# Optimization experiments

Hardware: AMD Instinct MI355X
Metric: run time of the kernel (lower is better)

Reference implementation:

```python
import jax, jax.numpy as jnp
import numpy as np

B, T, IN, H, NB, OUT = 256, 2048, 128, 256, 4, 8
BS = H // NB  # branch size = 64


def setup_inputs() -> dict:
    key = jax.random.key(0)
    ks = jax.random.split(key, 7)
    x = jax.random.normal(ks[0], (B, T, IN), dtype=jnp.float32)
    Wb = jax.random.normal(ks[1], (NB, IN, BS), dtype=jnp.float32) * (1.0 / np.sqrt(IN))
    bb = jax.random.normal(ks[2], (NB, BS), dtype=jnp.float32) * 0.05
    Wo = jax.random.normal(ks[3], (H, OUT), dtype=jnp.float32) * (1.0 / np.sqrt(H))
    bo = jax.random.normal(ks[4], (OUT,), dtype=jnp.float32) * 0.05
    # tau_m ~ U(0,4); tau_n branch i ~ U(-4+2i, -1+2i) per the torch init
    tau_m = jax.random.uniform(ks[5], (H,), dtype=jnp.float32, minval=0.0, maxval=4.0)
    lo = (-4.0 + 2.0 * jnp.arange(NB, dtype=jnp.float32))[:, None]
    tau_n = lo + 3.0 * jax.random.uniform(ks[6], (NB, BS), dtype=jnp.float32)
    return {"x": x, "Wb": Wb, "bb": bb, "Wo": Wo, "bo": bo,
            "tau_m": tau_m, "tau_n": tau_n}


def reference(x, Wb, bb, Wo, bo, tau_m, tau_n):
    Bsz = x.shape[0]
    # Batch all per-step branch projections into one einsum: [B,T,NB,BS] -> [B,T,H]
    # (branch i writes slice [i*BS:(i+1)*BS], which matches the reshape order)
    D = jnp.einsum('bti,nis->btns', x, Wb) + bb  # [B,T,NB,BS]
    D = D.reshape(Bsz, x.shape[1], -1)           # [B,T,H]

    beta = jax.nn.sigmoid(tau_n).reshape(-1)     # [H], per-branch smoothing
    alpha = jax.nn.sigmoid(tau_m)                # [H]

    def step(carry, d_t):
        c, m = carry
        c = beta * c + (1.0 - beta) * d_t        # dendritic current EMA
        m = alpha * m + (1.0 - alpha) * c        # membrane EMA
        o = jax.nn.sigmoid(m @ Wo + bo)          # [B,OUT]
        return (c, m), o

    init = (jnp.zeros((Bsz, D.shape[-1]), D.dtype),
            jnp.zeros((Bsz, D.shape[-1]), D.dtype))
    _, outs = jax.lax.scan(step, init, jnp.swapaxes(D, 0, 1))  # outs: [T,B,OUT]
    return jnp.swapaxes(outs, 0, 1)              # [B,T,OUT]
```

## Files before the change

kernel.cpp:

```cpp
#include <hip/hip_runtime.h>
#include <hip/hip_bf16.h>
#include <math.h>

#define DEVFN __device__ __forceinline__

typedef __attribute__((ext_vector_type(8))) __bf16 bf16x8;
typedef __attribute__((ext_vector_type(8))) short s16x8;
typedef __attribute__((ext_vector_type(4))) float f32x4;
typedef __attribute__((ext_vector_type(4))) unsigned int u32x4;

constexpr int Tt    = 2048;
constexpr int INt   = 128;
constexpr int Ht    = 256;
constexpr int OUTt  = 8;
constexpr int TT    = 32;
constexpr int NTILE = 64;

union Frag {
  s16x8 s;
  bf16x8 b;
  u32x4 u;
};

DEVFN unsigned short f2bf(float f) {
  unsigned int u = __builtin_bit_cast(unsigned int, f);
  u += 0x7fffu + ((u >> 16) & 1u);
  return (unsigned short)(u >> 16);
}

DEVFN unsigned int pack2(float lo, float hi) {
  return (unsigned int)f2bf(lo) | ((unsigned int)f2bf(hi) << 16);
}

__global__
__attribute__((amdgpu_flat_work_group_size(1024, 1024)))
void sfnn_fused(
    const float* __restrict__ x, const float* __restrict__ Wb,
    const float* __restrict__ bb, const float* __restrict__ Wo,
    const float* __restrict__ bo, const float* __restrict__ tau_m,
    const float* __restrict__ tau_n, float* __restrict__ out)
{
  const int b    = blockIdx.x;
  const int tid  = threadIdx.x;
  const int lane = tid & 63;
  const int w    = tid >> 6;
  const int l16  = lane & 15;
  const int lhi  = lane >> 4;
  const int sid  = tid - 512;

  __shared__ __align__(16) unsigned char  Xb[3][TT * 256];
  __shared__ __align__(16) float          DfT[2][Ht * TT];
  __shared__ __align__(16) unsigned short Mb[2][TT * Ht];
  __shared__ __align__(16) unsigned short WoT[16 * Ht];

  {
    const int j  = w;
    const int k0 = 4 * (tid & 63);
    float v0 = 0.f, v1 = 0.f, v2 = 0.f, v3 = 0.f;
    if (j < OUTt) {
      v0 = Wo[(k0 + 0) * OUTt + j]; v1 = Wo[(k0 + 1) * OUTt + j];
      v2 = Wo[(k0 + 2) * OUTt + j]; v3 = Wo[(k0 + 3) * OUTt + j];
    }
    unsigned long long pk = (unsigned long long)pack2(v0, v1) |
                            ((unsigned long long)pack2(v2, v3) << 32);
    *(unsigned long long*)(&WoT[j * 256 + (k0 ^ ((j & 7) << 3))]) = pk;
  }

  Frag Wf[4];
  {
    const int h = 16 * w + l16;
    const int n = h >> 6, s = h & 63;
    #pragma unroll
    for (int ks = 0; ks < 4; ++ks) {
      #pragma unroll
      for (int j = 0; j < 8; ++j) {
        const int i = 32 * ks + 8 * lhi + j;
        Wf[ks].s[j] = (short)f2bf(Wb[(n * 128 + i) * 64 + s]);
      }
    }
  }

  float beta = 0.f, alpha = 0.f, omb = 0.f, oma = 0.f, bbh = 0.f;
  if (tid < 256) {
    beta  = 1.f / (1.f + expf(-tau_n[tid]));
    alpha = 1.f / (1.f + expf(-tau_m[tid]));
    omb   = 1.f - beta;
    oma   = 1.f - alpha;
    bbh   = bb[tid];
  }
  float bo_l = 0.f;
  if (w == 4 || w == 5) bo_l = (l16 < OUTt) ? bo[l16] : 0.f;

  const float* xb   = x   + (size_t)b * Tt * INt;
  float*       outb = out + (size_t)b * Tt * OUTt;

  float c_s = 0.f, m_s = 0.f;
  f32x4 dacc[2];
  f32x4 QA0, QA1, QB0, QB1;

  #define BAR() do {                                                       \
    asm volatile("s_waitcnt lgkmcnt(0)" ::: "memory");                     \
    __builtin_amdgcn_s_barrier();                                          \
  } while (0)

  #define WAITVM(N) do {                                                   \
    asm volatile("s_waitcnt vmcnt(" #N ")" ::: "memory");                  \
    __builtin_amdgcn_sched_barrier(0);                                     \
  } while (0)

  #define ISSUE(TILE, Q0, Q1) do {                                         \
    const float* _p = xb + (size_t)(TILE) * (TT * INt) + 4 * (size_t)sid;  \
    asm volatile("global_load_dwordx4 %0, %1, off" : "=&v"(Q0) : "v"(_p));        \
    asm volatile("global_load_dwordx4 %0, %1, off" : "=&v"(Q1) : "v"(_p + 2048)); \
  } while (0)

  #define STAGEWR(BUF, Q0, Q1) do {                                        \
    const int kb = 8 * (sid & 31);                                         \
    {                                                                      \
      const int t = (sid >> 5);                                            \
      unsigned long long pk = (unsigned long long)pack2(Q0.x, Q0.y) |      \
            ((unsigned long long)pack2(Q0.z, Q0.w) << 32);                 \
      *(unsigned long long*)(&Xb[BUF][t * 256 + (kb ^ ((t & 7) << 4))]) = pk; \
    }                                                                      \
    {                                                                      \
      const int t = 16 + (sid >> 5);                                       \
      unsigned long long pk = (unsigned long long)pack2(Q1.x, Q1.y) |      \
            ((unsigned long long)pack2(Q1.z, Q1.w) << 32);                 \
      *(unsigned long long*)(&Xb[BUF][t * 256 + (kb ^ ((t & 7) << 4))]) = pk; \
    }                                                                      \
  } while (0)

  #define GEMM(BUF) do {                                                   \
    _Pragma("unroll")                                                      \
    for (int tt = 0; tt < 2; ++tt) {                                       \
      dacc[tt] = f32x4{0.f, 0.f, 0.f, 0.f};                                \
      const int row = 16 * tt + l16;                                       \
      const int rs = row * 256, sw = (row & 7) << 4;                       \
      _Pragma("unroll")                                                    \
      for (int ks = 0; ks < 4; ++ks) {                                     \
        Frag a;                                                            \
        a.u = *(const u32x4*)(&Xb[BUF][rs + ((64 * ks + 16 * lhi) ^ sw)]); \
        dacc[tt] = __builtin_amdgcn_mfma_f32_16x16x32_bf16(                \
            a.b, Wf[ks].b, dacc[tt], 0, 0, 0);                             \
      }                                                                    \
    }                                                                      \
  } while (0)

  #define WRITEDF(BUF) do {                                                \
    const int h = 16 * w + l16;                                            \
    _Pragma("unroll")                                                      \
    for (int tt = 0; tt < 2; ++tt) {                                       \
      const int qi = 4 * tt + lhi;                                         \
      *(f32x4*)(&DfT[BUF][h * 32 + ((qi ^ (h & 7)) << 2)]) = dacc[tt];     \
    }                                                                      \
  } while (0)

  #define SCAN(BUF) do {                                                   \
    if (tid < 256) {                                                       \
      const int hb = tid * 32, h7 = tid & 7;                               \
      _Pragma("unroll")                                                    \
      for (int g = 0; g < 2; ++g) {                                        \
        f32x4 dv[4];                                                       \
        _Pragma("unroll")                                                  \
        for (int q = 0; q < 4; ++q)                                        \
          dv[q] = *(const f32x4*)(&DfT[BUF][hb + (((4 * g + q) ^ h7) << 2)]); \
        _Pragma("unroll")                                                  \
        for (int q = 0; q < 4; ++q)                                        \
          _Pragma("unroll")                                                \
          for (int r = 0; r < 4; ++r) {                                    \
            const int t = 16 * g + 4 * q + r;                              \
            const float d = dv[q][r] + bbh;                                \
            c_s = fmaf(beta, c_s, omb * d);                                \
            m_s = fmaf(alpha, m_s, oma * c_s);                             \
            Mb[BUF][t * 256 + (tid ^ ((t & 7) << 3))] = f2bf(m_s);         \
          }                                                                \
      }                                                                    \
    }                                                                      \
  } while (0)

  #define PROJ(TI, BUF) do {                                               \
    const int tp = w - 4;                                                  \
    const int trow = 16 * tp + l16;                                        \
    const int mrb = trow * 256, msw = (trow & 7) << 3;                     \
    const int wrb = l16 * 256,  wsw = (l16 & 7) << 3;                      \
    f32x4 p = f32x4{0.f, 0.f, 0.f, 0.f};                                   \
    _Pragma("unroll")                                                      \
    for (int ks = 0; ks < 8; ++ks) {                                       \
      const int k0 = 32 * ks + 8 * lhi;                                    \
      Frag ma, wo;                                                         \
      ma.u = *(const u32x4*)(&Mb[BUF][mrb + (k0 ^ msw)]);                  \
      wo.u = *(const u32x4*)(&WoT[wrb + (k0 ^ wsw)]);                      \
      p = __builtin_amdgcn_mfma_f32_16x16x32_bf16(ma.b, wo.b, p, 0, 0, 0); \
    }                                                                      \
    if (l16 < OUTt) {                                                      \
      _Pragma("unroll")                                                    \
      for (int r = 0; r < 4; ++r) {                                        \
        const int t = 16 * tp + 4 * lhi + r;                               \
        outb[(size_t)((TI) * TT + t) * OUTt + l16] =                       \
            1.f / (1.f + __expf(-(p[r] + bo_l)));                          \
      }                                                                    \
    }                                                                      \
  } while (0)

  #define ITER_EV(I, DOG, DOS, DOP, DOISS, DOSTG, WN) do {                 \
    if ((DOISS) && w >= 8) ISSUE((I) + 2, QA0, QA1);                       \
    if (DOG) { GEMM((I) % 3); WRITEDF((I) & 1); }                          \
    if ((DOS) && w < 4) SCAN(((I) - 1) & 1);                               \
    if ((DOP) && (w == 4 || w == 5)) PROJ((I) - 2, (I) & 1);               \
    if ((DOSTG) && w >= 8) { WAITVM(WN); STAGEWR(((I) + 1) % 3, QB0, QB1); } \
    BAR();                                                                 \
  } while (0)

  #define ITER_OD(I, DOG, DOS, DOP, DOISS, DOSTG, WN) do {                 \
    if ((DOISS) && w >= 8) ISSUE((I) + 2, QB0, QB1);                       \
    if (DOG) { GEMM((I) % 3); WRITEDF((I) & 1); }                          \
    if ((DOS) && w < 4) SCAN(((I) - 1) & 1);                               \
    if ((DOP) && (w == 4 || w == 5)) PROJ((I) - 2, (I) & 1);               \
    if ((DOSTG) && w >= 8) { WAITVM(WN); STAGEWR(((I) + 1) % 3, QA0, QA1); } \
    BAR();                                                                 \
  } while (0)

  if (w >= 8) {
    ISSUE(0, QA0, QA1);
    WAITVM(0);
    STAGEWR(0, QA0, QA1);
    ISSUE(1, QB0, QB1);
  }
  BAR();

  ITER_EV(0, 1, 0, 0, 1, 1, 2);
  ITER_OD(1, 1, 1, 0, 1, 1, 2);
  for (int jj = 1; jj <= 30; ++jj) {
    ITER_EV(2 * jj,     1, 1, 1, 1, 1, 2);
    ITER_OD(2 * jj + 1, 1, 1, 1, 1, 1, 2);
  }
  ITER_EV(62, 1, 1, 1, 0, 1, 0);
  ITER_OD(63, 1, 1, 1, 0, 0, 0);
  ITER_EV(64, 0, 1, 1, 0, 0, 0);
  ITER_OD(65, 0, 0, 1, 0, 0, 0);

  #undef ISSUE
  #undef STAGEWR
  #undef GEMM
  #undef WRITEDF
  #undef SCAN
  #undef PROJ
  #undef ITER_EV
  #undef ITER_OD
  #undef BAR
  #undef WAITVM
}

extern "C" void kernel_launch(void* const* d_in, const int* in_sizes, int n_in,
                              void* d_out, int out_size, void* d_ws, size_t ws_size,
                              hipStream_t stream) {
  const float* x     = (const float*)d_in[0];
  const float* Wb    = (const float*)d_in[1];
  const float* bb    = (const float*)d_in[2];
  const float* Wo    = (const float*)d_in[3];
  const float* bo    = (const float*)d_in[4];
  const float* tau_m = (const float*)d_in[5];
  const float* tau_n = (const float*)d_in[6];
  float* out = (float*)d_out;

  sfnn_fused<<<dim3(256), dim3(1024), 0, stream>>>(x, Wb, bb, Wo, bo, tau_m, tau_n, out);
}
```

Measured before the change: 96.59 us.

## Stream x tiles via direct-to-LDS DMA and specialize waves by role

Two dedicated loader waves now copy raw fp32 x tiles straight into a double-buffered LDS staging area with global_load_lds. They then convert each tile to swizzled bf16 in a separate LDS buffer. The GEMM moves off all 16 waves onto 8 waves, each computing two 16-column N tiles with reused A fragments, and the Xb ring drops from three buffers to two. The aim is to cut register-staged loads and per-wave overhead, and to separate scan, projection, GEMM and loading into disjoint wave roles. In exchange, LDS use rises to about 152KB and global load bandwidth depends on only two waves.

```diff
diff --git a/kernel.cpp b/kernel.cpp
--- a/kernel.cpp
+++ b/kernel.cpp
@@ -30,6 +30,15 @@
 
 DEVFN unsigned int pack2(float lo, float hi) {
   return (unsigned int)f2bf(lo) | ((unsigned int)f2bf(hi) << 16);
+}
+
+typedef __attribute__((address_space(3))) unsigned int lds_u32;
+typedef const __attribute__((address_space(1))) unsigned int glb_u32;
+
+DEVFN void dma16(const float* g, const float* l) {
+  __builtin_amdgcn_global_load_lds((glb_u32*)(uintptr_t)g,
+                                   (lds_u32*)(unsigned int)(uintptr_t)l,
+                                   16, 0, 0);
 }
 
 __global__
@@ -46,9 +55,12 @@
   const int w    = tid >> 6;
   const int l16  = lane & 15;
   const int lhi  = lane >> 4;
-  const int sid  = tid - 512;
-
-  __shared__ __align__(16) unsigned char  Xb[3][TT * 256];
+
+  const int hg  = w - 6;
+  const int sw2 = w - 14;
+
+  __shared__ __align__(16) float          Xraw[2][TT * INt];
+  __shared__ __align__(16) unsigned char  Xb[2][TT * 256];
   __shared__ __align__(16) float          DfT[2][Ht * TT];
   __shared__ __align__(16) unsigned short Mb[2][TT * Ht];
   __shared__ __align__(16) unsigned short WoT[16 * Ht];
@@ -66,16 +78,19 @@
     *(unsigned long long*)(&WoT[j * 256 + (k0 ^ ((j & 7) << 3))]) = pk;
   }
 
-  Frag Wf[4];
-  {
-    const int h = 16 * w + l16;
-    const int n = h >> 6, s = h & 63;
+  Frag Wf[2][4];
+  if (w >= 6 && w < 14) {
     #pragma unroll
-    for (int ks = 0; ks < 4; ++ks) {
+    for (int nh = 0; nh < 2; ++nh) {
+      const int h = 32 * hg + 16 * nh + l16;
+      const int n = h >> 6, s = h & 63;
       #pragma unroll
-      for (int j = 0; j < 8; ++j) {
-        const int i = 32 * ks + 8 * lhi + j;
-        Wf[ks].s[j] = (short)f2bf(Wb[(n * 128 + i) * 64 + s]);
+      for (int ks = 0; ks < 4; ++ks) {
+        #pragma unroll
+        for (int j = 0; j < 8; ++j) {
+          const int i = 32 * ks + 8 * lhi + j;
+          Wf[nh][ks].s[j] = (short)f2bf(Wb[(n * 128 + i) * 64 + s]);
+        }
       }
     }
   }
@@ -95,8 +110,7 @@
   float*       outb = out + (size_t)b * Tt * OUTt;
 
   float c_s = 0.f, m_s = 0.f;
-  f32x4 dacc[2];
-  f32x4 QA0, QA1, QB0, QB1;
+  f32x4 dacc[2][2];
 
   #define BAR() do {                                                       \
     asm volatile("s_waitcnt lgkmcnt(0)" ::: "memory");                     \
@@ -108,50 +122,58 @@
     __builtin_amdgcn_sched_barrier(0);                                     \
   } while (0)
 
-  #define ISSUE(TILE, Q0, Q1) do {                                         \
-    const float* _p = xb + (size_t)(TILE) * (TT * INt) + 4 * (size_t)sid;  \
-    asm volatile("global_load_dwordx4 %0, %1, off" : "=&v"(Q0) : "v"(_p));        \
-    asm volatile("global_load_dwordx4 %0, %1, off" : "=&v"(Q1) : "v"(_p + 2048)); \
-  } while (0)
-
-  #define STAGEWR(BUF, Q0, Q1) do {                                        \
-    const int kb = 8 * (sid & 31);                                         \
-    {                                                                      \
-      const int t = (sid >> 5);                                            \
-      unsigned long long pk = (unsigned long long)pack2(Q0.x, Q0.y) |      \
-            ((unsigned long long)pack2(Q0.z, Q0.w) << 32);                 \
-      *(unsigned long long*)(&Xb[BUF][t * 256 + (kb ^ ((t & 7) << 4))]) = pk; \
-    }                                                                      \
-    {                                                                      \
-      const int t = 16 + (sid >> 5);                                       \
-      unsigned long long pk = (unsigned long long)pack2(Q1.x, Q1.y) |      \
-            ((unsigned long long)pack2(Q1.z, Q1.w) << 32);                 \
-      *(unsigned long long*)(&Xb[BUF][t * 256 + (kb ^ ((t & 7) << 4))]) = pk; \
+  #define ISSUE_DMA(TILE) do {                                             \
+    const int _bi = (TILE) & 1;                                            \
+    const float* _gs = xb + (size_t)(TILE) * (TT * INt);                   \
+    _Pragma("unroll")                                                      \
+    for (int q = 0; q < 8; ++q) {                                          \
+      const int c = 8 * sw2 + q;                                           \
+      dma16(_gs + c * 256 + lane * 4, &Xraw[_bi][c * 256]);                \
+    }                                                                      \
+  } while (0)
+
+  #define CONVERT(TILE) do {                                               \
+    const int _bi = (TILE) & 1;                                            \
+    const int kb  = 8 * (lane & 31);                                       \
+    _Pragma("unroll")                                                      \
+    for (int q = 0; q < 8; ++q) {                                          \
+      const int c = 8 * sw2 + q;                                           \
+      const int t = 2 * c + (lane >> 5);                                   \
+      f32x4 v = *(const f32x4*)(&Xraw[_bi][256 * c + 4 * lane]);           \
+      unsigned long long pk = (unsigned long long)pack2(v[0], v[1]) |      \
+            ((unsigned long long)pack2(v[2], v[3]) << 32);                 \
+      *(unsigned long long*)(&Xb[_bi][t * 256 + (kb ^ ((t & 7) << 4))]) = pk; \
     }                                                                      \
   } while (0)
 
   #define GEMM(BUF) do {                                                   \
     _Pragma("unroll")                                                      \
     for (int tt = 0; tt < 2; ++tt) {                                       \
-      dacc[tt] = f32x4{0.f, 0.f, 0.f, 0.f};                                \
+      _Pragma("unroll")                                                    \
+      for (int nh = 0; nh < 2; ++nh) dacc[tt][nh] = f32x4{0.f,0.f,0.f,0.f};\
       const int row = 16 * tt + l16;                                       \
       const int rs = row * 256, sw = (row & 7) << 4;                       \
       _Pragma("unroll")                                                    \
       for (int ks = 0; ks < 4; ++ks) {                                     \
         Frag a;                                                            \
         a.u = *(const u32x4*)(&Xb[BUF][rs + ((64 * ks + 16 * lhi) ^ sw)]); \
-        dacc[tt] = __builtin_amdgcn_mfma_f32_16x16x32_bf16(                \
-            a.b, Wf[ks].b, dacc[tt], 0, 0, 0);                             \
+        _Pragma("unroll")                                                  \
+        for (int nh = 0; nh < 2; ++nh)                                     \
+          dacc[tt][nh] = __builtin_amdgcn_mfma_f32_16x16x32_bf16(          \
+              a.b, Wf[nh][ks].b, dacc[tt][nh], 0, 0, 0);                   \
       }                                                                    \
     }                                                                      \
   } while (0)
 
   #define WRITEDF(BUF) do {                                                \
-    const int h = 16 * w + l16;                                            \
     _Pragma("unroll")                                                      \
     for (int tt = 0; tt < 2; ++tt) {                                       \
       const int qi = 4 * tt + lhi;                                         \
-      *(f32x4*)(&DfT[BUF][h * 32 + ((qi ^ (h & 7)) << 2)]) = dacc[tt];     \
+      _Pragma("unroll")                                                    \
+      for (int nh = 0; nh < 2; ++nh) {                                     \
+        const int h = 32 * hg + 16 * nh + l16;                             \
+        *(f32x4*)(&DfT[BUF][h * 32 + ((qi ^ (h & 7)) << 2)]) = dacc[tt][nh]; \
+      }                                                                    \
     }                                                                      \
   } while (0)
 
@@ -202,51 +224,38 @@
     }                                                                      \
   } while (0)
 
-  #define ITER_EV(I, DOG, DOS, DOP, DOISS, DOSTG, WN) do {                 \
-    if ((DOISS) && w >= 8) ISSUE((I) + 2, QA0, QA1);                       \
-    if (DOG) { GEMM((I) % 3); WRITEDF((I) & 1); }                          \
-    if ((DOS) && w < 4) SCAN(((I) - 1) & 1);                               \
-    if ((DOP) && (w == 4 || w == 5)) PROJ((I) - 2, (I) & 1);               \
-    if ((DOSTG) && w >= 8) { WAITVM(WN); STAGEWR(((I) + 1) % 3, QB0, QB1); } \
+  #define ITER(I, DOG, DOS, DOP, ISS_STMT, WAIT_STMT, CVT_STMT) do {       \
+    if (w < 4)        { if (DOS) SCAN(((I) - 1) & 1); }                    \
+    else if (w < 6)   { if (DOP) PROJ((I) - 2, (I) & 1); }                 \
+    else if (w < 14)  { if (DOG) { GEMM((I) & 1); WRITEDF((I) & 1); } }    \
+    else              { ISS_STMT; WAIT_STMT; CVT_STMT; }                   \
     BAR();                                                                 \
   } while (0)
 
-  #define ITER_OD(I, DOG, DOS, DOP, DOISS, DOSTG, WN) do {                 \
-    if ((DOISS) && w >= 8) ISSUE((I) + 2, QB0, QB1);                       \
-    if (DOG) { GEMM((I) % 3); WRITEDF((I) & 1); }                          \
-    if ((DOS) && w < 4) SCAN(((I) - 1) & 1);                               \
-    if ((DOP) && (w == 4 || w == 5)) PROJ((I) - 2, (I) & 1);               \
-    if ((DOSTG) && w >= 8) { WAITVM(WN); STAGEWR(((I) + 1) % 3, QA0, QA1); } \
-    BAR();                                                                 \
-  } while (0)
-
-  if (w >= 8) {
-    ISSUE(0, QA0, QA1);
-    WAITVM(0);
-    STAGEWR(0, QA0, QA1);
-    ISSUE(1, QB0, QB1);
+  if (w >= 14) {
+    ISSUE_DMA(0);
+    ISSUE_DMA(1);
+    WAITVM(8);
+    CONVERT(0);
   }
   BAR();
 
-  ITER_EV(0, 1, 0, 0, 1, 1, 2);
-  ITER_OD(1, 1, 1, 0, 1, 1, 2);
-  for (int jj = 1; jj <= 30; ++jj) {
-    ITER_EV(2 * jj,     1, 1, 1, 1, 1, 2);
-    ITER_OD(2 * jj + 1, 1, 1, 1, 1, 1, 2);
-  }
-  ITER_EV(62, 1, 1, 1, 0, 1, 0);
-  ITER_OD(63, 1, 1, 1, 0, 0, 0);
-  ITER_EV(64, 0, 1, 1, 0, 0, 0);
-  ITER_OD(65, 0, 0, 1, 0, 0, 0);
-
-  #undef ISSUE
-  #undef STAGEWR
+  ITER(0, 1, 0, 0, ISSUE_DMA(2), WAITVM(8), CONVERT(1));
+  ITER(1, 1, 1, 0, ISSUE_DMA(3), WAITVM(8), CONVERT(2));
+  for (int I = 2; I <= 61; ++I)
+    ITER(I, 1, 1, 1, ISSUE_DMA(I + 2), WAITVM(8), CONVERT(I + 1));
+  ITER(62, 1, 1, 1, (void)0, WAITVM(0), CONVERT(63));
+  ITER(63, 1, 1, 1, (void)0, (void)0, (void)0);
+  ITER(64, 0, 1, 1, (void)0, (void)0, (void)0);
+  ITER(65, 0, 0, 1, (void)0, (void)0, (void)0);
+
+  #undef ISSUE_DMA
+  #undef CONVERT
   #undef GEMM
   #undef WRITEDF
   #undef SCAN
   #undef PROJ
-  #undef ITER_EV
-  #undef ITER_OD
+  #undef ITER
   #undef BAR
   #undef WAITVM
 }
```

After: 117.0 us. 21.1% more time.
